# Kernel tuning notes

Hardware: AMD Instinct MI355X
Metric: run time of the kernel (lower is better)

The kernel has to match this reference:

```python
import jax, jax.numpy as jnp
import numpy as np

B, S, D, H = 2, 2048, 1024, 16


def setup_inputs() -> dict:
    key = jax.random.key(0)
    kq, kk, kv1, kv2 = jax.random.split(key, 4)
    return {
        "q": jax.random.normal(kq, (B, S, D), dtype=jnp.float32),
        "k": jax.random.normal(kk, (B, S, D), dtype=jnp.float32),
        "v1": jax.random.normal(kv1, (B, S, D), dtype=jnp.float32),
        "v2": jax.random.normal(kv2, (B, S, D), dtype=jnp.float32),
        "num_attn_heads": 16,
    }


def _split_heads(x, h):
    b, s, d = x.shape
    return x.reshape(b, s, h, d // h).transpose(0, 2, 1, 3)  # [B,H,S,dh]


def reference(q, k, v1, v2, num_attn_heads):
    h = num_attn_heads
    b, s, d = q.shape
    dh = d // h
    qh = _split_heads(q, h)
    kh = _split_heads(k, h)
    v1h = _split_heads(v1, h)
    v2h = _split_heads(v2, h)
    scores = jnp.einsum("bhqd,bhkd->bhqk", qh, kh) / jnp.sqrt(jnp.float32(dh))
    # Faithful to create_mask(input, 0): nopeek = triu(ones, k=0); mask = (nopeek == 0)
    # -> only STRICTLY lower triangle is visible; diagonal and above get -1e9.
    # Row 0 is fully masked -> softmax uniform (same as torch behavior).
    allowed = jnp.tril(jnp.ones((s, s), dtype=bool), k=-1)  # [S,S] j < i
    scores = jnp.where(allowed[None, None], scores, jnp.float32(-1e9))
    p_attn = jax.nn.softmax(scores, axis=-1)  # dropout p=0.0 -> identity
    o1 = jnp.einsum("bhqk,bhkd->bhqd", p_attn, v1h)
    o2 = jnp.einsum("bhqk,bhkd->bhqd", p_attn, v2h)
    o1 = o1.transpose(0, 2, 1, 3).reshape(b, s, d)
    o2 = o2.transpose(0, 2, 1, 3).reshape(b, s, d)
    return (o1, o2)
```

## Files before the change

### kernel.cpp

```cpp
#include <hip/hip_runtime.h>

#define B_ 2
#define S_ 2048
#define D_ 1024
#define H_ 16
#define DH 64
#define OFF2 (B_ * S_ * D_)
#define ELEMS (B_ * H_ * S_ * DH)

typedef __attribute__((ext_vector_type(8))) __bf16 bf16x8;
typedef __attribute__((ext_vector_type(4))) float f32x4;
typedef __attribute__((ext_vector_type(4))) unsigned int u32x4;
typedef __attribute__((ext_vector_type(2))) unsigned int u32x2;
typedef __attribute__((address_space(3))) unsigned int lds_u32;
typedef __attribute__((address_space(1))) const unsigned int glob_u32;

__device__ __forceinline__ unsigned short f2bf(float f) {
    return __builtin_bit_cast(unsigned short, (__bf16)f);
}
__device__ __forceinline__ unsigned int pk2(float a, float b) {
    return (unsigned int)f2bf(a) | ((unsigned int)f2bf(b) << 16);
}
__device__ __forceinline__ float bf2f(unsigned short h) {
    unsigned int u = ((unsigned int)h) << 16;
    return __builtin_bit_cast(float, u);
}

__global__ void prep_all(const float* __restrict__ k,
                         const float* __restrict__ v1, const float* __restrict__ v2,
                         unsigned short* __restrict__ kb,
                         unsigned short* __restrict__ v1t, unsigned short* __restrict__ v2t) {
    int id = blockIdx.x;
    if (id < 2048) {
        int cid = id * 256 + threadIdx.x;
        int d8 = cid & 7;
        int s  = (cid >> 3) & (S_ - 1);
        int h  = (cid >> 14) & (H_ - 1);
        int b  = cid >> 18;
        int off = (b * S_ + s) * D_ + h * DH + d8 * 8;
        float4 f0 = *(const float4*)(k + off);
        float4 f1 = *(const float4*)(k + off + 4);
        u32x4 wv = {pk2(f0.x, f0.y), pk2(f0.z, f0.w),
                    pk2(f1.x, f1.y), pk2(f1.z, f1.w)};
        *(u32x4*)(kb + cid * 8) = wv;
        return;
    }
    __shared__ __align__(16) unsigned short ldsT[64][72];
    int id2 = id - 2048;
    int t = threadIdx.x;
    int s0 = (id2 & 31) * 64;
    int bh = (id2 >> 5) & 31;
    int b = bh >> 4, h = bh & 15;
    const float* src = (id2 >> 10) ? v2 : v1;
    unsigned short* dst = (id2 >> 10) ? v2t : v1t;
    {
        int sl = t >> 2, dc = t & 3;
        int off = (b * S_ + s0 + sl) * D_ + h * DH + dc * 16;
#pragma unroll
        for (int i4 = 0; i4 < 4; i4++) {
            float4 f = *(const float4*)(src + off + i4 * 4);
            int d = dc * 16 + i4 * 4;
            ldsT[d + 0][sl] = f2bf(f.x);
            ldsT[d + 1][sl] = f2bf(f.y);
            ldsT[d + 2][sl] = f2bf(f.z);
            ldsT[d + 3][sl] = f2bf(f.w);
        }
    }
    __syncthreads();
    {
        int d = t >> 2, sc = t & 3;
        u32x4 a = *(const u32x4*)(&ldsT[d][sc * 16]);
        u32x4 c = *(const u32x4*)(&ldsT[d][sc * 16 + 8]);
        int off = (bh * DH + d) * S_ + s0 + sc * 16;
        *(u32x4*)(dst + off) = a;
        *(u32x4*)(dst + off + 8) = c;
    }
}

__global__ __launch_bounds__(256) void flash_attn(
        const float* __restrict__ qf, const unsigned short* __restrict__ kb,
        const unsigned short* __restrict__ v1t, const unsigned short* __restrict__ v2t,
        float* __restrict__ out) {
    __shared__ __align__(16) unsigned short sK0[4096], sK1[4096];
    __shared__ __align__(16) unsigned short sV1[4096], sV2[4096];

    int tid = threadIdx.x;
    int w = tid >> 6, lane = tid & 63;
    int lr = lane & 15, lg = lane >> 4;
    int srow = tid >> 3, sco = tid & 7;

    int id = blockIdx.x;
    int xcd = id & 7;
    int j = id >> 3;
    int bh = xcd * 4 + (j & 3);
    int qt = 31 - (j >> 2);
    int b = bh >> 4, hh = bh & 15;

    const unsigned short* gK  = kb  + bh * (S_ * DH);
    const unsigned short* gV1 = v1t + bh * (DH * S_);
    const unsigned short* gV2 = v2t + bh * (DH * S_);

    auto stageV = [&](int t) {
#pragma unroll
        for (int jj = 0; jj < 2; jj++) {
            int row = srow + jj * 32;
            int cosw = (sco ^ (row & 7)) * 8;
            int c8 = (tid + jj * 256) * 8;
            __builtin_amdgcn_global_load_lds((glob_u32*)(gV1 + row * S_ + t * 64 + cosw),
                                             (lds_u32*)(sV1 + c8), 16, 0, 0);
            __builtin_amdgcn_global_load_lds((glob_u32*)(gV2 + row * S_ + t * 64 + cosw),
                                             (lds_u32*)(sV2 + c8), 16, 0, 0);
        }
    };
    auto stageK = [&](unsigned short* dK, int t) {
#pragma unroll
        for (int jj = 0; jj < 2; jj++) {
            int row = srow + jj * 32;
            int cosw = (sco ^ (row & 7)) * 8;
            int c8 = (tid + jj * 256) * 8;
            __builtin_amdgcn_global_load_lds((glob_u32*)(gK + (t * 64 + row) * 64 + cosw),
                                             (lds_u32*)(dK + c8), 16, 0, 0);
        }
    };

    bf16x8 qa[2];
    {
        const float qs = 0.125f * 1.4426950408889634f;
        const float* a = qf + ((size_t)b * S_ + qt * 64 + w * 16 + lr) * D_ + hh * DH + lg * 8;
        float4 q0 = *(const float4*)a;
        float4 q1 = *(const float4*)(a + 4);
        float4 q2 = *(const float4*)(a + 32);
        float4 q3 = *(const float4*)(a + 36);
        u32x4 w0 = {pk2(q0.x * qs, q0.y * qs), pk2(q0.z * qs, q0.w * qs),
                    pk2(q1.x * qs, q1.y * qs), pk2(q1.z * qs, q1.w * qs)};
        u32x4 w1 = {pk2(q2.x * qs, q2.y * qs), pk2(q2.z * qs, q2.w * qs),
                    pk2(q3.x * qs, q3.y * qs), pk2(q3.z * qs, q3.w * qs)};
        qa[0] = __builtin_bit_cast(bf16x8, w0);
        qa[1] = __builtin_bit_cast(bf16x8, w1);
    }

    const u32x4 onesu = {0x3F803F80u, 0x3F803F80u, 0x3F803F80u, 0x3F803F80u};
    const bf16x8 ones = __builtin_bit_cast(bf16x8, onesu);

    f32x4 acc1[4], acc2[4], lacc;
#pragma unroll
    for (int dt = 0; dt < 4; dt++) {
        acc1[dt] = (f32x4){0.f, 0.f, 0.f, 0.f};
        acc2[dt] = (f32x4){0.f, 0.f, 0.f, 0.f};
    }
    lacc = (f32x4){0.f, 0.f, 0.f, 0.f};

    auto iterBody = [&](int t, const unsigned short* cK, bool last) {
        f32x4 s[4];
        __builtin_amdgcn_s_setprio(1);
#pragma unroll
        for (int n = 0; n < 4; n++) {
            int kv = n * 16 + lr;
            int ix0 = ((kv << 6) + lg * 8) ^ ((kv & 7) << 3);
            int ix1 = ((kv << 6) + 32 + lg * 8) ^ ((kv & 7) << 3);
            bf16x8 k0 = __builtin_bit_cast(bf16x8, *(const u32x4*)(cK + ix0));
            bf16x8 k1 = __builtin_bit_cast(bf16x8, *(const u32x4*)(cK + ix1));
            f32x4 a = __builtin_amdgcn_mfma_f32_16x16x32_bf16(
                k0, qa[0], (f32x4){-20.f, -20.f, -20.f, -20.f}, 0, 0, 0);
            s[n] = __builtin_amdgcn_mfma_f32_16x16x32_bf16(k1, qa[1], a, 0, 0, 0);
        }
        __builtin_amdgcn_s_setprio(0);
        if (last) {
#pragma unroll
            for (int n = 0; n < 4; n++)
#pragma unroll
                for (int r = 0; r < 4; r++)
                    if (n * 16 + lg * 4 + r >= w * 16 + lr) s[n][r] = -1e30f;
        }
        u32x4 pa[2];
#pragma unroll
        for (int ks = 0; ks < 2; ks++) {
            float p0[4], p1[4];
#pragma unroll
            for (int r = 0; r < 4; r++) {
                p0[r] = __builtin_amdgcn_exp2f(s[2 * ks][r]);
                p1[r] = __builtin_amdgcn_exp2f(s[2 * ks + 1][r]);
            }
            unsigned int u0 = pk2(p0[0], p0[1]);
            unsigned int u1 = pk2(p0[2], p0[3]);
            unsigned int u2 = pk2(p1[0], p1[1]);
            unsigned int u3 = pk2(p1[2], p1[3]);
            u32x2 ab = __builtin_amdgcn_permlane32_swap(u0, u2, false, false);
            u32x2 cd = __builtin_amdgcn_permlane32_swap(u1, u3, false, false);
            u32x2 ab2 = __builtin_amdgcn_permlane16_swap(ab[0], ab[1], false, false);
            u32x2 cd2 = __builtin_amdgcn_permlane16_swap(cd[0], cd[1], false, false);
            pa[ks] = (u32x4){ab2[0], cd2[0], ab2[1], cd2[1]};
        }
        if (last) asm volatile("s_waitcnt vmcnt(0)" ::: "memory");
        else      asm volatile("s_waitcnt vmcnt(2)" ::: "memory");
        __builtin_amdgcn_s_barrier();
        __builtin_amdgcn_s_setprio(1);
#pragma unroll
        for (int ks = 0; ks < 2; ks++) {
            bf16x8 pab = __builtin_bit_cast(bf16x8, pa[ks]);
            lacc = __builtin_amdgcn_mfma_f32_16x16x32_bf16(ones, pab, lacc, 0, 0, 0);
#pragma unroll
            for (int dt = 0; dt < 4; dt++) {
                int d = dt * 16 + lr;
                int vix = ((d << 6) + ks * 32 + lg * 8) ^ ((d & 7) << 3);
                bf16x8 vf1 = __builtin_bit_cast(bf16x8, *(const u32x4*)(sV1 + vix));
                acc1[dt] = __builtin_amdgcn_mfma_f32_16x16x32_bf16(vf1, pab, acc1[dt], 0, 0, 0);
                bf16x8 vf2 = __builtin_bit_cast(bf16x8, *(const u32x4*)(sV2 + vix));
                acc2[dt] = __builtin_amdgcn_mfma_f32_16x16x32_bf16(vf2, pab, acc2[dt], 0, 0, 0);
            }
        }
        __builtin_amdgcn_s_setprio(0);
    };

    stageK(sK0, 0);
    int t = 0;
    for (; t < qt; t++) {
        const unsigned short* cK = (t & 1) ? sK1 : sK0;
        unsigned short* nK       = (t & 1) ? sK0 : sK1;
        __builtin_amdgcn_s_barrier();
        stageV(t);
        stageK(nK, t + 1);
        asm volatile("s_waitcnt vmcnt(6)" ::: "memory");
        iterBody(t, cK, false);
    }
    {
        const unsigned short* cK = (t & 1) ? sK1 : sK0;
        __builtin_amdgcn_s_barrier();
        stageV(t);
        asm volatile("s_waitcnt vmcnt(4)" ::: "memory");
        iterBody(t, cK, true);
    }

    float inv = 1.0f / lacc[0];
    {
        int qrow = qt * 64 + w * 16 + lr;
        int base = (b * S_ + qrow) * D_ + hh * DH + lg * 4;
#pragma unroll
        for (int dt = 0; dt < 4; dt++) {
            f32x4 o1 = acc1[dt] * inv;
            f32x4 o2 = acc2[dt] * inv;
            *(f32x4*)(out + base + dt * 16) = o1;
            *(f32x4*)(out + base + dt * 16 + OFF2) = o2;
        }
    }
}

__global__ void row0_mean(const unsigned short* __restrict__ v1t,
                          const unsigned short* __restrict__ v2t,
                          float* __restrict__ out) {
    int wid = blockIdx.x * 4 + (threadIdx.x >> 6);
    int lane = threadIdx.x & 63;
    int tz = wid >> 11;
    int bhd = wid & 2047;
    const unsigned short* src = (tz ? v2t : v1t) + bhd * S_;
    float sum = 0.f;
#pragma unroll
    for (int kk = 0; kk < 4; kk++) {
        u32x4 v = *(const u32x4*)(src + (kk * 64 + lane) * 8);
#pragma unroll
        for (int jj = 0; jj < 4; jj++) {
            unsigned int u = v[jj];
            sum += bf2f((unsigned short)(u & 0xffff)) + bf2f((unsigned short)(u >> 16));
        }
    }
#pragma unroll
    for (int msk = 32; msk >= 1; msk >>= 1) sum += __shfl_xor(sum, msk, 64);
    if (lane == 0) {
        int b = bhd >> 10, rem = bhd & 1023, h = rem >> 6, d = rem & 63;
        out[tz * OFF2 + b * (S_ * D_) + h * DH + d] = sum * (1.0f / S_);
    }
}

extern "C" void kernel_launch(void* const* d_in, const int* in_sizes, int n_in,
                              void* d_out, int out_size, void* d_ws, size_t ws_size,
                              hipStream_t stream) {
    const float* q  = (const float*)d_in[0];
    const float* k  = (const float*)d_in[1];
    const float* v1 = (const float*)d_in[2];
    const float* v2 = (const float*)d_in[3];
    float* out = (float*)d_out;

    unsigned short* kb  = (unsigned short*)d_ws;
    unsigned short* v1t = kb + ELEMS;
    unsigned short* v2t = v1t + ELEMS;

    prep_all<<<4096, 256, 0, stream>>>(k, v1, v2, kb, v1t, v2t);
    flash_attn<<<1024, 256, 0, stream>>>(q, kb, v1t, v2t, out);
    row0_mean<<<1024, 256, 0, stream>>>(v1t, v2t, out);
}
```

Baseline: 66.88 us.

## Fuse row-0 mean into prep kernel, snake-order q-tiles, unify attention loop

The separate row0_mean kernel is removed. Its per-column sums are now computed during the V transpose in prep_all through DPP reductions and atomicAdd into an output row that is zeroed by memsets. The flash_attn block-to-qtile mapping changes from a plain descending order to a serpentine order across rounds, to balance causal work per XCD slot. The peeled last iteration is folded into one loop with a redundant K stage. The change also adds four memset launches and float atomics, so the summation order becomes nondeterministic.

```diff
diff --git a/kernel.cpp b/kernel.cpp
--- a/kernel.cpp
+++ b/kernel.cpp
@@ -26,10 +26,17 @@
     return __builtin_bit_cast(float, u);
 }
 
+template <int CTRL>
+__device__ __forceinline__ float dpp_mov(float x) {
+    return __builtin_bit_cast(float, __builtin_amdgcn_update_dpp(
+        0, __builtin_bit_cast(int, x), CTRL, 0xf, 0xf, false));
+}
+
 __global__ void prep_all(const float* __restrict__ k,
                          const float* __restrict__ v1, const float* __restrict__ v2,
                          unsigned short* __restrict__ kb,
-                         unsigned short* __restrict__ v1t, unsigned short* __restrict__ v2t) {
+                         unsigned short* __restrict__ v1t, unsigned short* __restrict__ v2t,
+                         float* __restrict__ out) {
     int id = blockIdx.x;
     if (id < 2048) {
         int cid = id * 256 + threadIdx.x;
@@ -51,8 +58,9 @@
     int s0 = (id2 & 31) * 64;
     int bh = (id2 >> 5) & 31;
     int b = bh >> 4, h = bh & 15;
-    const float* src = (id2 >> 10) ? v2 : v1;
-    unsigned short* dst = (id2 >> 10) ? v2t : v1t;
+    int tz = id2 >> 10;
+    const float* src = tz ? v2 : v1;
+    unsigned short* dst = tz ? v2t : v1t;
     {
         int sl = t >> 2, dc = t & 3;
         int off = (b * S_ + s0 + sl) * D_ + h * DH + dc * 16;
@@ -74,6 +82,16 @@
         int off = (bh * DH + d) * S_ + s0 + sc * 16;
         *(u32x4*)(dst + off) = a;
         *(u32x4*)(dst + off + 8) = c;
+        float sum = 0.f;
+#pragma unroll
+        for (int jj = 0; jj < 4; jj++) {
+            sum += bf2f((unsigned short)(a[jj] & 0xffff)) + bf2f((unsigned short)(a[jj] >> 16));
+            sum += bf2f((unsigned short)(c[jj] & 0xffff)) + bf2f((unsigned short)(c[jj] >> 16));
+        }
+        sum += dpp_mov<0xB1>(sum);
+        sum += dpp_mov<0x4E>(sum);
+        if (sc == 0)
+            atomicAdd(&out[tz * OFF2 + b * (S_ * D_) + h * DH + d], sum * (1.0f / S_));
     }
 }
 
@@ -92,8 +110,10 @@
     int id = blockIdx.x;
     int xcd = id & 7;
     int j = id >> 3;
-    int bh = xcd * 4 + (j & 3);
-    int qt = 31 - (j >> 2);
+    int r = j >> 5, s5 = j & 31;
+    int c = s5 >> 2;
+    int bh = xcd * 4 + (s5 & 3);
+    int qt = (r == 0) ? 31 - c : (r == 1) ? 16 + c : (r == 2) ? 15 - c : c;
     int b = bh >> 4, hh = bh & 15;
 
     const unsigned short* gK  = kb  + bh * (S_ * DH);
@@ -150,7 +170,15 @@
     }
     lacc = (f32x4){0.f, 0.f, 0.f, 0.f};
 
-    auto iterBody = [&](int t, const unsigned short* cK, bool last) {
+    stageK(sK0, 0);
+
+    for (int t = 0; t <= qt; t++) {
+        const unsigned short* cK = (t & 1) ? sK1 : sK0;
+        unsigned short* nK       = (t & 1) ? sK0 : sK1;
+        __builtin_amdgcn_s_barrier();
+        stageV(t);
+        stageK(nK, (t < qt) ? t + 1 : qt);
+        asm volatile("s_waitcnt vmcnt(6)" ::: "memory");
         f32x4 s[4];
         __builtin_amdgcn_s_setprio(1);
 #pragma unroll
@@ -165,21 +193,21 @@
             s[n] = __builtin_amdgcn_mfma_f32_16x16x32_bf16(k1, qa[1], a, 0, 0, 0);
         }
         __builtin_amdgcn_s_setprio(0);
-        if (last) {
+        if (t == qt) {
 #pragma unroll
             for (int n = 0; n < 4; n++)
 #pragma unroll
-                for (int r = 0; r < 4; r++)
-                    if (n * 16 + lg * 4 + r >= w * 16 + lr) s[n][r] = -1e30f;
+                for (int rr = 0; rr < 4; rr++)
+                    if (n * 16 + lg * 4 + rr >= w * 16 + lr) s[n][rr] = -1e30f;
         }
         u32x4 pa[2];
 #pragma unroll
         for (int ks = 0; ks < 2; ks++) {
             float p0[4], p1[4];
 #pragma unroll
-            for (int r = 0; r < 4; r++) {
-                p0[r] = __builtin_amdgcn_exp2f(s[2 * ks][r]);
-                p1[r] = __builtin_amdgcn_exp2f(s[2 * ks + 1][r]);
+            for (int rr = 0; rr < 4; rr++) {
+                p0[rr] = __builtin_amdgcn_exp2f(s[2 * ks][rr]);
+                p1[rr] = __builtin_amdgcn_exp2f(s[2 * ks + 1][rr]);
             }
             unsigned int u0 = pk2(p0[0], p0[1]);
             unsigned int u1 = pk2(p0[2], p0[3]);
@@ -191,8 +219,7 @@
             u32x2 cd2 = __builtin_amdgcn_permlane16_swap(cd[0], cd[1], false, false);
             pa[ks] = (u32x4){ab2[0], cd2[0], ab2[1], cd2[1]};
         }
-        if (last) asm volatile("s_waitcnt vmcnt(0)" ::: "memory");
-        else      asm volatile("s_waitcnt vmcnt(2)" ::: "memory");
+        asm volatile("s_waitcnt vmcnt(2)" ::: "memory");
         __builtin_amdgcn_s_barrier();
         __builtin_amdgcn_s_setprio(1);
 #pragma unroll
@@ -210,30 +237,13 @@
             }
         }
         __builtin_amdgcn_s_setprio(0);
-    };
-
-    stageK(sK0, 0);
-    int t = 0;
-    for (; t < qt; t++) {
-        const unsigned short* cK = (t & 1) ? sK1 : sK0;
-        unsigned short* nK       = (t & 1) ? sK0 : sK1;
-        __builtin_amdgcn_s_barrier();
-        stageV(t);
-        stageK(nK, t + 1);
-        asm volatile("s_waitcnt vmcnt(6)" ::: "memory");
-        iterBody(t, cK, false);
-    }
-    {
-        const unsigned short* cK = (t & 1) ? sK1 : sK0;
-        __builtin_amdgcn_s_barrier();
-        stageV(t);
-        asm volatile("s_waitcnt vmcnt(4)" ::: "memory");
-        iterBody(t, cK, true);
-    }
+    }
+
+    asm volatile("s_waitcnt vmcnt(0)" ::: "memory");
 
     float inv = 1.0f / lacc[0];
-    {
-        int qrow = qt * 64 + w * 16 + lr;
+    int qrow = qt * 64 + w * 16 + lr;
+    if (qrow != 0) {
         int base = (b * S_ + qrow) * D_ + hh * DH + lg * 4;
 #pragma unroll
         for (int dt = 0; dt < 4; dt++) {
@@ -242,32 +252,6 @@
             *(f32x4*)(out + base + dt * 16) = o1;
             *(f32x4*)(out + base + dt * 16 + OFF2) = o2;
         }
-    }
-}
-
-__global__ void row0_mean(const unsigned short* __restrict__ v1t,
-                          const unsigned short* __restrict__ v2t,
-                          float* __restrict__ out) {
-    int wid = blockIdx.x * 4 + (threadIdx.x >> 6);
-    int lane = threadIdx.x & 63;
-    int tz = wid >> 11;
-    int bhd = wid & 2047;
-    const unsigned short* src = (tz ? v2t : v1t) + bhd * S_;
-    float sum = 0.f;
-#pragma unroll
-    for (int kk = 0; kk < 4; kk++) {
-        u32x4 v = *(const u32x4*)(src + (kk * 64 + lane) * 8);
-#pragma unroll
-        for (int jj = 0; jj < 4; jj++) {
-            unsigned int u = v[jj];
-            sum += bf2f((unsigned short)(u & 0xffff)) + bf2f((unsigned short)(u >> 16));
-        }
-    }
-#pragma unroll
-    for (int msk = 32; msk >= 1; msk >>= 1) sum += __shfl_xor(sum, msk, 64);
-    if (lane == 0) {
-        int b = bhd >> 10, rem = bhd & 1023, h = rem >> 6, d = rem & 63;
-        out[tz * OFF2 + b * (S_ * D_) + h * DH + d] = sum * (1.0f / S_);
     }
 }
 
@@ -284,7 +268,10 @@
     unsigned short* v1t = kb + ELEMS;
     unsigned short* v2t = v1t + ELEMS;
 
-    prep_all<<<4096, 256, 0, stream>>>(k, v1, v2, kb, v1t, v2t);
+    for (int tz = 0; tz < 2; tz++)
+        for (int b = 0; b < 2; b++)
+            hipMemsetAsync(out + tz * OFF2 + b * (S_ * D_), 0, D_ * sizeof(float), stream);
+
+    prep_all<<<4096, 256, 0, stream>>>(k, v1, v2, kb, v1t, v2t, out);
     flash_attn<<<1024, 256, 0, stream>>>(q, kb, v1t, v2t, out);
-    row0_mean<<<1024, 256, 0, stream>>>(v1t, v2t, out);
-}
+}
```

Result: slower. 74.85 us (+11.9%).
